# Optimization experiments

Measured on AMD Instinct MI355X. Metric: run time of the kernel, lower is better.

Reference implementation:

```python
import jax, jax.numpy as jnp
import numpy as np

CONF_THRES = 0.96
IOU_THRES = 0.45
MAX_CAND = 2048        # fixed candidate cap (jit-static stand-in for data-dependent nonzero)
DET_PER_IMG = 300
AGNOSTIC = False
LABEL_OFF = 4.0        # class offset for batched NMS; boxes lie within [-0.5, 1.5]


def _cxcywh_to_xyxy(b):
    cx, cy, w, h = b[..., 0], b[..., 1], b[..., 2], b[..., 3]
    return jnp.stack([cx - 0.5 * w, cy - 0.5 * h, cx + 0.5 * w, cy + 0.5 * h], axis=-1)


def _box_iou(a, b):
    # a: [K,4], b: [K,4] -> [K,K]
    lt = jnp.maximum(a[:, None, :2], b[None, :, :2])
    rb = jnp.minimum(a[:, None, 2:], b[None, :, 2:])
    wh = jnp.clip(rb - lt, 0.0)
    inter = wh[..., 0] * wh[..., 1]
    area_a = (a[:, 2] - a[:, 0]) * (a[:, 3] - a[:, 1])
    area_b = (b[:, 2] - b[:, 0]) * (b[:, 3] - b[:, 1])
    return inter / (area_a[:, None] + area_b[None, :] - inter + 1e-9)


def _process_image(x, nc):
    # x: [N, 5+nc]
    obj = x[:, 4]
    cls_scores = x[:, 5:] * obj[:, None]                 # x[:,5:] *= x[:,4:5]
    boxes = _cxcywh_to_xyxy(x[:, :4])                    # [N,4]
    # multi-label candidates: (obj > conf) pre-filter, then (obj*cls > conf)
    cand_mask = (cls_scores > CONF_THRES) & (obj[:, None] > CONF_THRES)
    flat_scores = jnp.where(cand_mask, cls_scores, -1.0).reshape(-1)  # [N*nc]
    top_scores, top_idx = jax.lax.top_k(flat_scores, MAX_CAND)        # sorted desc
    anchor = top_idx // nc
    label = top_idx % nc
    cand_boxes = boxes[anchor]                           # [K,4]
    valid = top_scores > 0.0

    # batched (class-aware) NMS via per-class coordinate offset
    if AGNOSTIC:
        nms_boxes = cand_boxes
    else:
        nms_boxes = cand_boxes + (label.astype(cand_boxes.dtype) * LABEL_OFF)[:, None]
    iou = _box_iou(nms_boxes, nms_boxes)                 # [K,K]
    idxs = jnp.arange(MAX_CAND)

    def body(i, keep):
        suppress = keep[i] & (iou[i] > IOU_THRES) & (idxs > i)
        return keep & ~suppress

    keep = jax.lax.fori_loop(0, MAX_CAND, body, valid)
    kept_scores = jnp.where(keep, top_scores, -1.0)
    det_scores, det_idx = jax.lax.top_k(kept_scores, DET_PER_IMG)
    det_valid = det_scores > 0.0
    det = jnp.concatenate(
        [cand_boxes[det_idx], det_scores[:, None], label[det_idx].astype(x.dtype)[:, None]],
        axis=1,
    )  # [DET_PER_IMG, 6] = (x1, y1, x2, y2, score, class)
    return jnp.where(det_valid[:, None], det, 0.0)


def setup_inputs() -> dict:
    key = jax.random.key(0)
    prediction = jax.random.uniform(key, (8, 25200, 85), dtype=jnp.float32)
    return {"prediction": prediction}


def reference(prediction):
    nc = prediction.shape[2] - 5
    return jax.vmap(lambda x: _process_image(x, nc))(prediction)
```

## Files before the change

kernel.cpp:

```cpp
#include <hip/hip_runtime.h>
#include <stdint.h>

#define CONF 0.96f
#define IOUT 0.45f
#define NA 25200
#define DIM 85
#define NC 80
#define NIMG 8
#define NCAND 2048
#define CAPRAW 4096
#define NDET 300
#define CSTRIDE 32
#define CH 64
#define NCH (NCAND / CH)
#define NTPAIR ((NCH * (NCH + 1)) / 2)

#define APB 112
#define BCAP 256
__global__ __launch_bounds__(256) void k1_filter(
    const float* __restrict__ pred, int* __restrict__ cnt,
    float* __restrict__ raw_s, int* __restrict__ raw_f) {
    __shared__ float lds[APB * DIM];
    __shared__ float l_s[BCAP];
    __shared__ int   l_f[BCAP];
    __shared__ int   l_cnt, l_base;
    int tid = threadIdx.x;
    int img = blockIdx.y;
    int a0 = blockIdx.x * APB;
    if (tid == 0) l_cnt = 0;

    const float4* src = (const float4*)(pred + ((size_t)img * NA + a0) * DIM);
    float4* dst = (float4*)lds;
    for (int i = tid; i < (APB * DIM / 4); i += 256) dst[i] = src[i];
    __syncthreads();

    for (int it = 0; it < (APB * NC / 256); ++it) {
        int w = tid + it * 256;
        int al = w / NC;
        int c = w - al * NC;
        float obj = lds[al * DIM + 4];
        float s = lds[al * DIM + 5 + c] * obj;
        if (s > CONF && obj > CONF) {
            int p = atomicAdd(&l_cnt, 1);
            if (p < BCAP) { l_s[p] = s; l_f[p] = (a0 + al) * NC + c; }
        }
    }
    __syncthreads();
    int c = l_cnt; if (c > BCAP) c = BCAP;
    if (tid == 0) l_base = c ? atomicAdd(&cnt[img * CSTRIDE], c) : 0;
    __syncthreads();
    int base = l_base;
    for (int i = tid; i < c; i += 256) {
        int pos = base + i;
        if (pos < CAPRAW) {
            raw_s[img * CAPRAW + pos] = l_s[i];
            raw_f[img * CAPRAW + pos] = l_f[i];
        }
    }
}

__global__ __launch_bounds__(256) void k2_rank(
    const float* __restrict__ pred,
    const int* __restrict__ cnt, int* __restrict__ n_arr,
    const float* __restrict__ raw_s, const int* __restrict__ raw_f,
    float* __restrict__ score, int* __restrict__ label,
    float* __restrict__ ox1, float* __restrict__ oy1,
    float* __restrict__ ox2, float* __restrict__ oy2,
    float* __restrict__ area,
    float* __restrict__ rx1, float* __restrict__ ry1,
    float* __restrict__ rx2, float* __restrict__ ry2) {
    __shared__ uint64_t keys[CAPRAW];
    int img = blockIdx.y;
    int tid = threadIdx.x;
    int m = cnt[img * CSTRIDE]; if (m > CAPRAW) m = CAPRAW;
    if (blockIdx.x == 0 && tid == 0) n_arr[img] = m < NCAND ? m : NCAND;

    const float* rs = raw_s + img * CAPRAW;
    const int*   rf = raw_f + img * CAPRAW;
    for (int j = tid; j < CAPRAW; j += 256) {
        uint64_t k = 0;
        if (j < m)
            k = ((uint64_t)__float_as_uint(rs[j]) << 32) | (uint32_t)(~(uint32_t)rf[j]);
        keys[j] = k;
    }
    __syncthreads();
    if (blockIdx.x * 256 >= m) return;

    int idx = blockIdx.x * 256 + tid;
    bool valid = idx < m;
    uint64_t my = keys[idx];
    int mt = (m + 7) & ~7;
    int rank = 0;
#pragma unroll 8
    for (int j = 0; j < mt; ++j) rank += (keys[j] > my) ? 1 : 0;

    if (valid && rank < NCAND) {
        float s = __uint_as_float((uint32_t)(my >> 32));
        uint32_t myf = ~((uint32_t)my);
        int anchor = (int)(myf / NC);
        int lab = (int)(myf - (uint32_t)anchor * NC);
        const float* p = pred + ((size_t)img * NA + anchor) * DIM;
        float cx = p[0], cy = p[1], wv = p[2], hv = p[3];
        float x1 = cx - 0.5f * wv, y1 = cy - 0.5f * hv;
        float x2 = cx + 0.5f * wv, y2 = cy + 0.5f * hv;
        float off = (float)lab * 4.0f;
        size_t o = (size_t)img * NCAND + rank;
        score[o] = s; label[o] = lab;
        rx1[o] = x1; ry1[o] = y1; rx2[o] = x2; ry2[o] = y2;
        float o1 = x1 + off, o2 = y1 + off, o3 = x2 + off, o4 = y2 + off;
        ox1[o] = o1; oy1[o] = o2; ox2[o] = o3; oy2[o] = o4;
        area[o] = (o3 - o1) * (o4 - o2);
    }
}

__global__ __launch_bounds__(64) void k3_mask(
    const int* __restrict__ n_arr,
    const float* __restrict__ ox1, const float* __restrict__ oy1,
    const float* __restrict__ ox2, const float* __restrict__ oy2,
    const float* __restrict__ area, uint64_t* __restrict__ mask64) {
    int img = blockIdx.y;
    int n = n_arr[img];
    int p = blockIdx.x, ci = 0;
    while (p >= NCH - ci) { p -= NCH - ci; ++ci; }
    int cj = ci + p;
    if (ci * CH >= n) return;
    int t = threadIdx.x;
    size_t base = (size_t)img * NCAND;
    __shared__ float jx1[CH], jy1[CH], jx2[CH], jy2[CH], jar[CH];
    {
        int j = cj * CH + t;
        float x1 = 0.f, y1 = 0.f, x2 = 0.f, y2 = 0.f, ar = 0.f;
        if (j < n) {
            x1 = ox1[base + j]; y1 = oy1[base + j];
            x2 = ox2[base + j]; y2 = oy2[base + j]; ar = area[base + j];
        }
        jx1[t] = x1; jy1[t] = y1; jx2[t] = x2; jy2[t] = y2; jar[t] = ar;
    }
    __syncthreads();
    int i = ci * CH + t;
    float ax1 = 0.f, ay1 = 0.f, ax2 = 0.f, ay2 = 0.f, aar = 0.f;
    if (i < n) {
        ax1 = ox1[base + i]; ay1 = oy1[base + i];
        ax2 = ox2[base + i]; ay2 = oy2[base + i]; aar = area[base + i];
    }
    int jg0 = cj * CH;
    uint64_t w = 0;
#pragma unroll 8
    for (int jj = 0; jj < CH; ++jj) {
        float ltx = fmaxf(ax1, jx1[jj]), lty = fmaxf(ay1, jy1[jj]);
        float rbx = fminf(ax2, jx2[jj]), rby = fminf(ay2, jy2[jj]);
        float ww = fmaxf(rbx - ltx, 0.f), hh = fmaxf(rby - lty, 0.f);
        float inter = ww * hh;
        float iou = inter / (aar + jar[jj] - inter + 1e-9f);
        w |= (iou > IOUT && (jg0 + jj) > i) ? (1ull << jj) : 0ull;
    }
    mask64[(base + (size_t)i) * NCH + cj] = w;
}

__global__ void k4_scan(const int* __restrict__ n_arr,
                        const uint32_t* __restrict__ mask,
                        const float* __restrict__ score, const int* __restrict__ label,
                        const float* __restrict__ rx1, const float* __restrict__ ry1,
                        const float* __restrict__ rx2, const float* __restrict__ ry2,
                        float* __restrict__ out) {
    int img = blockIdx.x;
    int lane = threadIdx.x;
    int n = n_arr[img];
    size_t cbase = (size_t)img * NCAND;
    const uint32_t* rowp = mask + cbase * 64 + lane;
    float* outp = out + (size_t)img * NDET * 6;

    uint32_t removed = 0;
    int kcnt = 0;
    constexpr int PF = 32;
    uint32_t buf[PF];
#pragma unroll
    for (int k = 0; k < PF; ++k) buf[k] = rowp[(size_t)k * 64];
    for (int ib = 0; ib < n; ib += PF) {
#pragma unroll
        for (int k = 0; k < PF; ++k) {
            int i = ib + k;
            uint32_t row = buf[k];
            int pi = i + PF; if (pi > NCAND - 1) pi = NCAND - 1;
            buf[k] = rowp[(size_t)pi * 64];
            uint32_t w = (uint32_t)__builtin_amdgcn_readlane((int)removed, i >> 5);
            uint32_t kept = ((w >> (i & 31)) & 1u) ^ 1u;
            kcnt += (int)kept;
            removed |= row & (0u - kept);
        }
        if (kcnt >= NDET) break;
    }

    int j0 = lane << 5;
    uint32_t vmask = (j0 + 32 <= n) ? 0xffffffffu
                   : (j0 >= n ? 0u : ((1u << (n - j0)) - 1u));
    uint32_t keptw = ~removed & vmask;
    int cnt = __popc(keptw);
    int pre = cnt;
    for (int d = 1; d < 64; d <<= 1) {
        int tv = __shfl_up(pre, d);
        if (lane >= d) pre += tv;
    }
    int total = __shfl(pre, 63);
    int r = pre - cnt;
    uint32_t wv = keptw;
    while (wv) {
        int b = __builtin_ctz(wv);
        wv &= wv - 1;
        if (r >= NDET) break;
        int j = j0 + b;
        float* o = outp + (size_t)r * 6;
        o[0] = rx1[cbase + j]; o[1] = ry1[cbase + j];
        o[2] = rx2[cbase + j]; o[3] = ry2[cbase + j];
        o[4] = score[cbase + j]; o[5] = (float)label[cbase + j];
        ++r;
    }
    int nk = total < NDET ? total : NDET;
    for (int idx = nk * 6 + lane; idx < NDET * 6; idx += 64) outp[idx] = 0.0f;
}

extern "C" void kernel_launch(void* const* d_in, const int* in_sizes, int n_in,
                              void* d_out, int out_size, void* d_ws, size_t ws_size,
                              hipStream_t stream) {
    const float* pred = (const float*)d_in[0];
    float* out = (float*)d_out;
    char* w = (char*)d_ws;

    const size_t A_CNT = 0;
    const size_t A_N   = 1024;
    const size_t A_RS  = 1280;
    const size_t SZ_RAW = (size_t)NIMG * CAPRAW * 4;
    const size_t A_RF  = A_RS + SZ_RAW;
    const size_t SA    = A_RF + SZ_RAW;
    const size_t SZ_S  = (size_t)NIMG * NCAND * 4;

    int*   cnt   = (int*)(w + A_CNT);
    int*   n_arr = (int*)(w + A_N);
    float* raw_s = (float*)(w + A_RS);
    int*   raw_f = (int*)(w + A_RF);
    float* score = (float*)(w + SA + 0 * SZ_S);
    int*   label = (int*)(w + SA + 1 * SZ_S);
    float* ox1   = (float*)(w + SA + 2 * SZ_S);
    float* oy1   = (float*)(w + SA + 3 * SZ_S);
    float* ox2   = (float*)(w + SA + 4 * SZ_S);
    float* oy2   = (float*)(w + SA + 5 * SZ_S);
    float* area  = (float*)(w + SA + 6 * SZ_S);
    float* rx1   = (float*)(w + SA + 7 * SZ_S);
    float* ry1   = (float*)(w + SA + 8 * SZ_S);
    float* rx2   = (float*)(w + SA + 9 * SZ_S);
    float* ry2   = (float*)(w + SA + 10 * SZ_S);
    uint64_t* mask64 = (uint64_t*)(w + SA + 11 * SZ_S);
    uint32_t* mask32 = (uint32_t*)mask64;

    hipMemsetAsync(cnt, 0, NIMG * CSTRIDE * sizeof(int), stream);
    hipMemsetAsync(mask64, 0, (size_t)NIMG * NCAND * NCH * 8, stream);
    dim3 g1(NA / APB, NIMG);
    k1_filter<<<g1, 256, 0, stream>>>(pred, cnt, raw_s, raw_f);
    dim3 g2(CAPRAW / 256, NIMG);
    k2_rank<<<g2, 256, 0, stream>>>(pred, cnt, n_arr, raw_s, raw_f,
        score, label, ox1, oy1, ox2, oy2, area, rx1, ry1, rx2, ry2);
    dim3 g3(NTPAIR, NIMG);
    k3_mask<<<g3, CH, 0, stream>>>(n_arr, ox1, oy1, ox2, oy2, area, mask64);
    k4_scan<<<NIMG, 64, 0, stream>>>(n_arr, mask32, score, label,
        rx1, ry1, rx2, ry2, out);
}
```

Measured before the change: 180.1 us.

## Fuse four NMS kernels into one cooperative persistent kernel with grid syncs

Merges filter, rank, IoU-mask and scan stages into a single cooperative kernel of 256 persistent blocks, separated by grid-wide syncs. Mask tiles are distributed across waves, and every tile (including inactive ones) writes zeros, which replaces the large mask memset. This targets the fixed cost of several kernel launches and one big memset. In exchange it adds grid-sync overhead, and the filter and rank stages run on fewer resident blocks than the original wide grids.

```diff
diff --git a/kernel.cpp b/kernel.cpp
--- a/kernel.cpp
+++ b/kernel.cpp
@@ -1,5 +1,7 @@
 #include <hip/hip_runtime.h>
+#include <hip/hip_cooperative_groups.h>
 #include <stdint.h>
+namespace cg = cooperative_groups;
 
 #define CONF 0.96f
 #define IOUT 0.45f
@@ -13,210 +15,221 @@
 #define CSTRIDE 32
 #define CH 64
 #define NCH (NCAND / CH)
-#define NTPAIR ((NCH * (NCH + 1)) / 2)
-
 #define APB 112
+#define NT1 (NA / APB)
 #define BCAP 256
-__global__ __launch_bounds__(256) void k1_filter(
-    const float* __restrict__ pred, int* __restrict__ cnt,
-    float* __restrict__ raw_s, int* __restrict__ raw_f) {
-    __shared__ float lds[APB * DIM];
-    __shared__ float l_s[BCAP];
-    __shared__ int   l_f[BCAP];
-    __shared__ int   l_cnt, l_base;
+#define NBLK 256
+#define NTHR 256
+
+__global__ __launch_bounds__(NTHR) void mega(
+    const float* __restrict__ pred, float* __restrict__ out,
+    int* cnt, int* n_arr, float* raw_s, int* raw_f,
+    float* score, int* label,
+    float* ox1, float* oy1, float* ox2, float* oy2, float* area,
+    float* rx1, float* ry1, float* rx2, float* ry2,
+    uint64_t* mask64) {
+    cg::grid_group grid = cg::this_grid();
+    __shared__ alignas(16) unsigned char smem[40192];
     int tid = threadIdx.x;
-    int img = blockIdx.y;
-    int a0 = blockIdx.x * APB;
-    if (tid == 0) l_cnt = 0;
-
-    const float4* src = (const float4*)(pred + ((size_t)img * NA + a0) * DIM);
-    float4* dst = (float4*)lds;
-    for (int i = tid; i < (APB * DIM / 4); i += 256) dst[i] = src[i];
-    __syncthreads();
-
-    for (int it = 0; it < (APB * NC / 256); ++it) {
-        int w = tid + it * 256;
-        int al = w / NC;
-        int c = w - al * NC;
-        float obj = lds[al * DIM + 4];
-        float s = lds[al * DIM + 5 + c] * obj;
-        if (s > CONF && obj > CONF) {
-            int p = atomicAdd(&l_cnt, 1);
-            if (p < BCAP) { l_s[p] = s; l_f[p] = (a0 + al) * NC + c; }
-        }
-    }
-    __syncthreads();
-    int c = l_cnt; if (c > BCAP) c = BCAP;
-    if (tid == 0) l_base = c ? atomicAdd(&cnt[img * CSTRIDE], c) : 0;
-    __syncthreads();
-    int base = l_base;
-    for (int i = tid; i < c; i += 256) {
-        int pos = base + i;
-        if (pos < CAPRAW) {
-            raw_s[img * CAPRAW + pos] = l_s[i];
-            raw_f[img * CAPRAW + pos] = l_f[i];
-        }
-    }
-}
-
-__global__ __launch_bounds__(256) void k2_rank(
-    const float* __restrict__ pred,
-    const int* __restrict__ cnt, int* __restrict__ n_arr,
-    const float* __restrict__ raw_s, const int* __restrict__ raw_f,
-    float* __restrict__ score, int* __restrict__ label,
-    float* __restrict__ ox1, float* __restrict__ oy1,
-    float* __restrict__ ox2, float* __restrict__ oy2,
-    float* __restrict__ area,
-    float* __restrict__ rx1, float* __restrict__ ry1,
-    float* __restrict__ rx2, float* __restrict__ ry2) {
-    __shared__ uint64_t keys[CAPRAW];
-    int img = blockIdx.y;
-    int tid = threadIdx.x;
-    int m = cnt[img * CSTRIDE]; if (m > CAPRAW) m = CAPRAW;
-    if (blockIdx.x == 0 && tid == 0) n_arr[img] = m < NCAND ? m : NCAND;
-
-    const float* rs = raw_s + img * CAPRAW;
-    const int*   rf = raw_f + img * CAPRAW;
-    for (int j = tid; j < CAPRAW; j += 256) {
-        uint64_t k = 0;
-        if (j < m)
-            k = ((uint64_t)__float_as_uint(rs[j]) << 32) | (uint32_t)(~(uint32_t)rf[j]);
-        keys[j] = k;
-    }
-    __syncthreads();
-    if (blockIdx.x * 256 >= m) return;
-
-    int idx = blockIdx.x * 256 + tid;
-    bool valid = idx < m;
-    uint64_t my = keys[idx];
-    int mt = (m + 7) & ~7;
-    int rank = 0;
+    int blk = blockIdx.x;
+
+    {
+        float* tile = (float*)smem;
+        float* l_s  = (float*)(smem + 38080);
+        int*   l_f  = (int*)  (smem + 38080 + 1024);
+        int*   l_c  = (int*)  (smem + 38080 + 2048);
+        for (int t = blk; t < NT1 * NIMG; t += NBLK) {
+            int img = t / NT1;
+            int a0 = (t - img * NT1) * APB;
+            if (tid == 0) l_c[0] = 0;
+            __syncthreads();
+            const float4* src = (const float4*)(pred + ((size_t)img * NA + a0) * DIM);
+            float4* dst = (float4*)tile;
+            for (int i = tid; i < (APB * DIM / 4); i += NTHR) dst[i] = src[i];
+            __syncthreads();
+            for (int it = 0; it < (APB * NC / NTHR); ++it) {
+                int wI = tid + it * NTHR;
+                int al = wI / NC;
+                int c  = wI - al * NC;
+                float obj = tile[al * DIM + 4];
+                float s = tile[al * DIM + 5 + c] * obj;
+                if (s > CONF && obj > CONF) {
+                    int p = atomicAdd(&l_c[0], 1);
+                    if (p < BCAP) { l_s[p] = s; l_f[p] = (a0 + al) * NC + c; }
+                }
+            }
+            __syncthreads();
+            int c = l_c[0]; if (c > BCAP) c = BCAP;
+            if (tid == 0) l_c[1] = c ? atomicAdd(&cnt[img * CSTRIDE], c) : 0;
+            __syncthreads();
+            int base = l_c[1];
+            for (int i = tid; i < c; i += NTHR) {
+                int pos = base + i;
+                if (pos < CAPRAW) {
+                    raw_s[img * CAPRAW + pos] = l_s[i];
+                    raw_f[img * CAPRAW + pos] = l_f[i];
+                }
+            }
+            __syncthreads();
+        }
+    }
+    __threadfence();
+    grid.sync();
+
+    if (blk < NIMG * (CAPRAW / NTHR)) {
+        uint64_t* keys = (uint64_t*)smem;
+        int img = blk >> 4;
+        int unit = blk & 15;
+        int m = cnt[img * CSTRIDE]; if (m > CAPRAW) m = CAPRAW;
+        if (unit == 0 && tid == 0) n_arr[img] = m < NCAND ? m : NCAND;
+        const float* rs = raw_s + img * CAPRAW;
+        const int*   rf = raw_f + img * CAPRAW;
+        for (int j = tid; j < CAPRAW; j += NTHR) {
+            uint64_t k = 0;
+            if (j < m)
+                k = ((uint64_t)__float_as_uint(rs[j]) << 32) | (uint32_t)(~(uint32_t)rf[j]);
+            keys[j] = k;
+        }
+        __syncthreads();
+        if (unit * NTHR < m) {
+            int idx = unit * NTHR + tid;
+            bool valid = idx < m;
+            uint64_t my = keys[idx];
+            int mt = (m + 7) & ~7;
+            int rank = 0;
 #pragma unroll 8
-    for (int j = 0; j < mt; ++j) rank += (keys[j] > my) ? 1 : 0;
-
-    if (valid && rank < NCAND) {
-        float s = __uint_as_float((uint32_t)(my >> 32));
-        uint32_t myf = ~((uint32_t)my);
-        int anchor = (int)(myf / NC);
-        int lab = (int)(myf - (uint32_t)anchor * NC);
-        const float* p = pred + ((size_t)img * NA + anchor) * DIM;
-        float cx = p[0], cy = p[1], wv = p[2], hv = p[3];
-        float x1 = cx - 0.5f * wv, y1 = cy - 0.5f * hv;
-        float x2 = cx + 0.5f * wv, y2 = cy + 0.5f * hv;
-        float off = (float)lab * 4.0f;
-        size_t o = (size_t)img * NCAND + rank;
-        score[o] = s; label[o] = lab;
-        rx1[o] = x1; ry1[o] = y1; rx2[o] = x2; ry2[o] = y2;
-        float o1 = x1 + off, o2 = y1 + off, o3 = x2 + off, o4 = y2 + off;
-        ox1[o] = o1; oy1[o] = o2; ox2[o] = o3; oy2[o] = o4;
-        area[o] = (o3 - o1) * (o4 - o2);
-    }
-}
-
-__global__ __launch_bounds__(64) void k3_mask(
-    const int* __restrict__ n_arr,
-    const float* __restrict__ ox1, const float* __restrict__ oy1,
-    const float* __restrict__ ox2, const float* __restrict__ oy2,
-    const float* __restrict__ area, uint64_t* __restrict__ mask64) {
-    int img = blockIdx.y;
-    int n = n_arr[img];
-    int p = blockIdx.x, ci = 0;
-    while (p >= NCH - ci) { p -= NCH - ci; ++ci; }
-    int cj = ci + p;
-    if (ci * CH >= n) return;
-    int t = threadIdx.x;
-    size_t base = (size_t)img * NCAND;
-    __shared__ float jx1[CH], jy1[CH], jx2[CH], jy2[CH], jar[CH];
+            for (int j = 0; j < mt; ++j) rank += (keys[j] > my) ? 1 : 0;
+            if (valid && rank < NCAND) {
+                float s = __uint_as_float((uint32_t)(my >> 32));
+                uint32_t myf = ~((uint32_t)my);
+                int anchor = (int)(myf / NC);
+                int lab = (int)(myf - (uint32_t)anchor * NC);
+                const float* p = pred + ((size_t)img * NA + anchor) * DIM;
+                float cx = p[0], cy = p[1], wv = p[2], hv = p[3];
+                float x1 = cx - 0.5f * wv, y1 = cy - 0.5f * hv;
+                float x2 = cx + 0.5f * wv, y2 = cy + 0.5f * hv;
+                float off = (float)lab * 4.0f;
+                size_t o = (size_t)img * NCAND + rank;
+                score[o] = s; label[o] = lab;
+                rx1[o] = x1; ry1[o] = y1; rx2[o] = x2; ry2[o] = y2;
+                float o1 = x1 + off, o2 = y1 + off, o3 = x2 + off, o4 = y2 + off;
+                ox1[o] = o1; oy1[o] = o2; ox2[o] = o3; oy2[o] = o4;
+                area[o] = (o3 - o1) * (o4 - o2);
+            }
+        }
+    }
+    __threadfence();
+    grid.sync();
+
     {
-        int j = cj * CH + t;
-        float x1 = 0.f, y1 = 0.f, x2 = 0.f, y2 = 0.f, ar = 0.f;
-        if (j < n) {
-            x1 = ox1[base + j]; y1 = oy1[base + j];
-            x2 = ox2[base + j]; y2 = oy2[base + j]; ar = area[base + j];
-        }
-        jx1[t] = x1; jy1[t] = y1; jx2[t] = x2; jy2[t] = y2; jar[t] = ar;
-    }
-    __syncthreads();
-    int i = ci * CH + t;
-    float ax1 = 0.f, ay1 = 0.f, ax2 = 0.f, ay2 = 0.f, aar = 0.f;
-    if (i < n) {
-        ax1 = ox1[base + i]; ay1 = oy1[base + i];
-        ax2 = ox2[base + i]; ay2 = oy2[base + i]; aar = area[base + i];
-    }
-    int jg0 = cj * CH;
-    uint64_t w = 0;
+        int wv = tid >> 6, lane = tid & 63;
+        float* jx1 = (float*)smem + (wv * 5 + 0) * 64;
+        float* jy1 = (float*)smem + (wv * 5 + 1) * 64;
+        float* jx2 = (float*)smem + (wv * 5 + 2) * 64;
+        float* jy2 = (float*)smem + (wv * 5 + 3) * 64;
+        float* jar = (float*)smem + (wv * 5 + 4) * 64;
+        for (int it = 0; it < 8; ++it) {
+            int T = it * (NBLK * 4) + blk * 4 + wv;
+            int img = T >> 10;
+            int r = T & 1023;
+            int ci = r >> 5, cj = r & 31;
+            int n = n_arr[img];
+            size_t base = (size_t)img * NCAND;
+            bool active = (cj >= ci) && (ci * CH < n) && (cj * CH < n);
+            if (active) {
+                int j = cj * CH + lane;
+                float x1 = 0.f, y1 = 0.f, x2 = 0.f, y2 = 0.f, ar = 0.f;
+                if (j < n) {
+                    x1 = ox1[base + j]; y1 = oy1[base + j];
+                    x2 = ox2[base + j]; y2 = oy2[base + j]; ar = area[base + j];
+                }
+                jx1[lane] = x1; jy1[lane] = y1; jx2[lane] = x2;
+                jy2[lane] = y2; jar[lane] = ar;
+            }
+            __syncthreads();
+            uint64_t w = 0;
+            int i = ci * CH + lane;
+            if (active) {
+                float ax1 = 0.f, ay1 = 0.f, ax2 = 0.f, ay2 = 0.f, aar = 0.f;
+                if (i < n) {
+                    ax1 = ox1[base + i]; ay1 = oy1[base + i];
+                    ax2 = ox2[base + i]; ay2 = oy2[base + i]; aar = area[base + i];
+                }
+                int jg0 = cj * CH;
 #pragma unroll 8
-    for (int jj = 0; jj < CH; ++jj) {
-        float ltx = fmaxf(ax1, jx1[jj]), lty = fmaxf(ay1, jy1[jj]);
-        float rbx = fminf(ax2, jx2[jj]), rby = fminf(ay2, jy2[jj]);
-        float ww = fmaxf(rbx - ltx, 0.f), hh = fmaxf(rby - lty, 0.f);
-        float inter = ww * hh;
-        float iou = inter / (aar + jar[jj] - inter + 1e-9f);
-        w |= (iou > IOUT && (jg0 + jj) > i) ? (1ull << jj) : 0ull;
-    }
-    mask64[(base + (size_t)i) * NCH + cj] = w;
-}
-
-__global__ void k4_scan(const int* __restrict__ n_arr,
-                        const uint32_t* __restrict__ mask,
-                        const float* __restrict__ score, const int* __restrict__ label,
-                        const float* __restrict__ rx1, const float* __restrict__ ry1,
-                        const float* __restrict__ rx2, const float* __restrict__ ry2,
-                        float* __restrict__ out) {
-    int img = blockIdx.x;
-    int lane = threadIdx.x;
-    int n = n_arr[img];
-    size_t cbase = (size_t)img * NCAND;
-    const uint32_t* rowp = mask + cbase * 64 + lane;
-    float* outp = out + (size_t)img * NDET * 6;
-
-    uint32_t removed = 0;
-    int kcnt = 0;
-    constexpr int PF = 32;
-    uint32_t buf[PF];
+                for (int jj = 0; jj < CH; ++jj) {
+                    float ltx = fmaxf(ax1, jx1[jj]), lty = fmaxf(ay1, jy1[jj]);
+                    float rbx = fminf(ax2, jx2[jj]), rby = fminf(ay2, jy2[jj]);
+                    float ww = fmaxf(rbx - ltx, 0.f), hh = fmaxf(rby - lty, 0.f);
+                    float inter = ww * hh;
+                    float iou = inter / (aar + jar[jj] - inter + 1e-9f);
+                    w |= (iou > IOUT && (jg0 + jj) > i) ? (1ull << jj) : 0ull;
+                }
+            }
+            mask64[(base + (size_t)i) * NCH + cj] = w;
+            __syncthreads();
+        }
+    }
+    __threadfence();
+    grid.sync();
+
+    if (blk < NIMG && tid < 64) {
+        const uint32_t* mask = (const uint32_t*)mask64;
+        int img = blk;
+        int lane = tid;
+        int n = n_arr[img];
+        size_t cbase = (size_t)img * NCAND;
+        const uint32_t* rowp = mask + cbase * 64 + lane;
+        float* outp = out + (size_t)img * NDET * 6;
+
+        uint32_t removed = 0;
+        int kcnt = 0;
+        constexpr int PF = 32;
+        uint32_t buf[PF];
 #pragma unroll
-    for (int k = 0; k < PF; ++k) buf[k] = rowp[(size_t)k * 64];
-    for (int ib = 0; ib < n; ib += PF) {
+        for (int k = 0; k < PF; ++k) buf[k] = rowp[(size_t)k * 64];
+        for (int ib = 0; ib < n; ib += PF) {
 #pragma unroll
-        for (int k = 0; k < PF; ++k) {
-            int i = ib + k;
-            uint32_t row = buf[k];
-            int pi = i + PF; if (pi > NCAND - 1) pi = NCAND - 1;
-            buf[k] = rowp[(size_t)pi * 64];
-            uint32_t w = (uint32_t)__builtin_amdgcn_readlane((int)removed, i >> 5);
-            uint32_t kept = ((w >> (i & 31)) & 1u) ^ 1u;
-            kcnt += (int)kept;
-            removed |= row & (0u - kept);
-        }
-        if (kcnt >= NDET) break;
-    }
-
-    int j0 = lane << 5;
-    uint32_t vmask = (j0 + 32 <= n) ? 0xffffffffu
-                   : (j0 >= n ? 0u : ((1u << (n - j0)) - 1u));
-    uint32_t keptw = ~removed & vmask;
-    int cnt = __popc(keptw);
-    int pre = cnt;
-    for (int d = 1; d < 64; d <<= 1) {
-        int tv = __shfl_up(pre, d);
-        if (lane >= d) pre += tv;
-    }
-    int total = __shfl(pre, 63);
-    int r = pre - cnt;
-    uint32_t wv = keptw;
-    while (wv) {
-        int b = __builtin_ctz(wv);
-        wv &= wv - 1;
-        if (r >= NDET) break;
-        int j = j0 + b;
-        float* o = outp + (size_t)r * 6;
-        o[0] = rx1[cbase + j]; o[1] = ry1[cbase + j];
-        o[2] = rx2[cbase + j]; o[3] = ry2[cbase + j];
-        o[4] = score[cbase + j]; o[5] = (float)label[cbase + j];
-        ++r;
-    }
-    int nk = total < NDET ? total : NDET;
-    for (int idx = nk * 6 + lane; idx < NDET * 6; idx += 64) outp[idx] = 0.0f;
+            for (int k = 0; k < PF; ++k) {
+                int i = ib + k;
+                uint32_t row = buf[k];
+                int pi = i + PF; if (pi > NCAND - 1) pi = NCAND - 1;
+                buf[k] = rowp[(size_t)pi * 64];
+                uint32_t w = (uint32_t)__builtin_amdgcn_readlane((int)removed, i >> 5);
+                uint32_t kept = ((w >> (i & 31)) & 1u) ^ 1u;
+                kcnt += (int)kept;
+                removed |= row & (0u - kept);
+            }
+            if (kcnt >= NDET) break;
+        }
+
+        int j0 = lane << 5;
+        uint32_t vmask = (j0 + 32 <= n) ? 0xffffffffu
+                       : (j0 >= n ? 0u : ((1u << (n - j0)) - 1u));
+        uint32_t keptw = ~removed & vmask;
+        int cntk = __popc(keptw);
+        int pre = cntk;
+        for (int d = 1; d < 64; d <<= 1) {
+            int tv = __shfl_up(pre, d);
+            if (lane >= d) pre += tv;
+        }
+        int total = __shfl(pre, 63);
+        int r = pre - cntk;
+        uint32_t wvb = keptw;
+        while (wvb) {
+            int b = __builtin_ctz(wvb);
+            wvb &= wvb - 1;
+            if (r >= NDET) break;
+            int j = j0 + b;
+            float* o = outp + (size_t)r * 6;
+            o[0] = rx1[cbase + j]; o[1] = ry1[cbase + j];
+            o[2] = rx2[cbase + j]; o[3] = ry2[cbase + j];
+            o[4] = score[cbase + j]; o[5] = (float)label[cbase + j];
+            ++r;
+        }
+        int nk = total < NDET ? total : NDET;
+        for (int idx = nk * 6 + lane; idx < NDET * 6; idx += 64) outp[idx] = 0.0f;
+    }
 }
 
 extern "C" void kernel_launch(void* const* d_in, const int* in_sizes, int n_in,
@@ -250,17 +263,15 @@
     float* rx2   = (float*)(w + SA + 9 * SZ_S);
     float* ry2   = (float*)(w + SA + 10 * SZ_S);
     uint64_t* mask64 = (uint64_t*)(w + SA + 11 * SZ_S);
-    uint32_t* mask32 = (uint32_t*)mask64;
 
     hipMemsetAsync(cnt, 0, NIMG * CSTRIDE * sizeof(int), stream);
-    hipMemsetAsync(mask64, 0, (size_t)NIMG * NCAND * NCH * 8, stream);
-    dim3 g1(NA / APB, NIMG);
-    k1_filter<<<g1, 256, 0, stream>>>(pred, cnt, raw_s, raw_f);
-    dim3 g2(CAPRAW / 256, NIMG);
-    k2_rank<<<g2, 256, 0, stream>>>(pred, cnt, n_arr, raw_s, raw_f,
-        score, label, ox1, oy1, ox2, oy2, area, rx1, ry1, rx2, ry2);
-    dim3 g3(NTPAIR, NIMG);
-    k3_mask<<<g3, CH, 0, stream>>>(n_arr, ox1, oy1, ox2, oy2, area, mask64);
-    k4_scan<<<NIMG, 64, 0, stream>>>(n_arr, mask32, score, label,
-        rx1, ry1, rx2, ry2, out);
+
+    void* args[] = {
+        (void*)&pred, (void*)&out, (void*)&cnt, (void*)&n_arr,
+        (void*)&raw_s, (void*)&raw_f, (void*)&score, (void*)&label,
+        (void*)&ox1, (void*)&oy1, (void*)&ox2, (void*)&oy2, (void*)&area,
+        (void*)&rx1, (void*)&ry1, (void*)&rx2, (void*)&ry2, (void*)&mask64,
+    };
+    hipLaunchCooperativeKernel((const void*)mega, dim3(NBLK), dim3(NTHR),
+                               args, 0, stream);
 }
```

Result: slower. 372.5 us (+106.9%).

## Prefilter anchors by objectness and write full mask grid instead of memset

Applied to the files above, without the earlier changes.

The filter kernel first collects anchors whose objectness exceeds the threshold, then scores classes only for those anchors, skipping most per-class multiply-compare work. The IoU mask kernel now launches the full square tile grid and writes zeros for tiles that are below the diagonal or out of range, so the separate memset of the mask buffer is removed. The trade-off is more (mostly trivial) blocks in the mask kernel, plus an extra shared-memory atomic phase and barrier in the filter kernel.

```diff
diff --git a/kernel.cpp b/kernel.cpp
--- a/kernel.cpp
+++ b/kernel.cpp
@@ -13,34 +13,41 @@
 #define CSTRIDE 32
 #define CH 64
 #define NCH (NCAND / CH)
-#define NTPAIR ((NCH * (NCH + 1)) / 2)
 
 #define APB 112
 #define BCAP 256
 __global__ __launch_bounds__(256) void k1_filter(
     const float* __restrict__ pred, int* __restrict__ cnt,
     float* __restrict__ raw_s, int* __restrict__ raw_f) {
-    __shared__ float lds[APB * DIM];
+    __shared__ float tile[APB * DIM];
+    __shared__ int   hot[APB];
     __shared__ float l_s[BCAP];
     __shared__ int   l_f[BCAP];
-    __shared__ int   l_cnt, l_base;
+    __shared__ int   l_hot, l_cnt, l_base;
     int tid = threadIdx.x;
     int img = blockIdx.y;
     int a0 = blockIdx.x * APB;
-    if (tid == 0) l_cnt = 0;
+    if (tid == 0) { l_hot = 0; l_cnt = 0; }
 
     const float4* src = (const float4*)(pred + ((size_t)img * NA + a0) * DIM);
-    float4* dst = (float4*)lds;
+    float4* dst = (float4*)tile;
     for (int i = tid; i < (APB * DIM / 4); i += 256) dst[i] = src[i];
     __syncthreads();
 
-    for (int it = 0; it < (APB * NC / 256); ++it) {
-        int w = tid + it * 256;
-        int al = w / NC;
-        int c = w - al * NC;
-        float obj = lds[al * DIM + 4];
-        float s = lds[al * DIM + 5 + c] * obj;
-        if (s > CONF && obj > CONF) {
+    if (tid < APB) {
+        float obj = tile[tid * DIM + 4];
+        if (obj > CONF) { int p = atomicAdd(&l_hot, 1); hot[p] = tid; }
+    }
+    __syncthreads();
+    int nh = l_hot;
+    int items = nh * NC;
+    for (int w = tid; w < items; w += 256) {
+        int hi = w / NC;
+        int c = w - hi * NC;
+        int al = hot[hi];
+        float obj = tile[al * DIM + 4];
+        float s = tile[al * DIM + 5 + c] * obj;
+        if (s > CONF) {
             int p = atomicAdd(&l_cnt, 1);
             if (p < BCAP) { l_s[p] = s; l_f[p] = (a0 + al) * NC + c; }
         }
@@ -118,41 +125,40 @@
     const float* __restrict__ ox1, const float* __restrict__ oy1,
     const float* __restrict__ ox2, const float* __restrict__ oy2,
     const float* __restrict__ area, uint64_t* __restrict__ mask64) {
+    __shared__ float jx1[CH], jy1[CH], jx2[CH], jy2[CH], jar[CH];
     int img = blockIdx.y;
     int n = n_arr[img];
-    int p = blockIdx.x, ci = 0;
-    while (p >= NCH - ci) { p -= NCH - ci; ++ci; }
-    int cj = ci + p;
-    if (ci * CH >= n) return;
+    int ci = blockIdx.x >> 5, cj = blockIdx.x & 31;
     int t = threadIdx.x;
     size_t base = (size_t)img * NCAND;
-    __shared__ float jx1[CH], jy1[CH], jx2[CH], jy2[CH], jar[CH];
-    {
-        int j = cj * CH + t;
-        float x1 = 0.f, y1 = 0.f, x2 = 0.f, y2 = 0.f, ar = 0.f;
-        if (j < n) {
-            x1 = ox1[base + j]; y1 = oy1[base + j];
-            x2 = ox2[base + j]; y2 = oy2[base + j]; ar = area[base + j];
-        }
-        jx1[t] = x1; jy1[t] = y1; jx2[t] = x2; jy2[t] = y2; jar[t] = ar;
-    }
-    __syncthreads();
     int i = ci * CH + t;
-    float ax1 = 0.f, ay1 = 0.f, ax2 = 0.f, ay2 = 0.f, aar = 0.f;
-    if (i < n) {
-        ax1 = ox1[base + i]; ay1 = oy1[base + i];
-        ax2 = ox2[base + i]; ay2 = oy2[base + i]; aar = area[base + i];
-    }
-    int jg0 = cj * CH;
     uint64_t w = 0;
+    if (cj >= ci && ci * CH < n && cj * CH < n) {
+        {
+            int j = cj * CH + t;
+            float x1 = 0.f, y1 = 0.f, x2 = 0.f, y2 = 0.f, ar = 0.f;
+            if (j < n) {
+                x1 = ox1[base + j]; y1 = oy1[base + j];
+                x2 = ox2[base + j]; y2 = oy2[base + j]; ar = area[base + j];
+            }
+            jx1[t] = x1; jy1[t] = y1; jx2[t] = x2; jy2[t] = y2; jar[t] = ar;
+        }
+        __syncthreads();
+        float ax1 = 0.f, ay1 = 0.f, ax2 = 0.f, ay2 = 0.f, aar = 0.f;
+        if (i < n) {
+            ax1 = ox1[base + i]; ay1 = oy1[base + i];
+            ax2 = ox2[base + i]; ay2 = oy2[base + i]; aar = area[base + i];
+        }
+        int jg0 = cj * CH;
 #pragma unroll 8
-    for (int jj = 0; jj < CH; ++jj) {
-        float ltx = fmaxf(ax1, jx1[jj]), lty = fmaxf(ay1, jy1[jj]);
-        float rbx = fminf(ax2, jx2[jj]), rby = fminf(ay2, jy2[jj]);
-        float ww = fmaxf(rbx - ltx, 0.f), hh = fmaxf(rby - lty, 0.f);
-        float inter = ww * hh;
-        float iou = inter / (aar + jar[jj] - inter + 1e-9f);
-        w |= (iou > IOUT && (jg0 + jj) > i) ? (1ull << jj) : 0ull;
+        for (int jj = 0; jj < CH; ++jj) {
+            float ltx = fmaxf(ax1, jx1[jj]), lty = fmaxf(ay1, jy1[jj]);
+            float rbx = fminf(ax2, jx2[jj]), rby = fminf(ay2, jy2[jj]);
+            float ww = fmaxf(rbx - ltx, 0.f), hh = fmaxf(rby - lty, 0.f);
+            float inter = ww * hh;
+            float iou = inter / (aar + jar[jj] - inter + 1e-9f);
+            w |= (iou > IOUT && (jg0 + jj) > i) ? (1ull << jj) : 0ull;
+        }
     }
     mask64[(base + (size_t)i) * NCH + cj] = w;
 }
@@ -195,14 +201,14 @@
     uint32_t vmask = (j0 + 32 <= n) ? 0xffffffffu
                    : (j0 >= n ? 0u : ((1u << (n - j0)) - 1u));
     uint32_t keptw = ~removed & vmask;
-    int cnt = __popc(keptw);
-    int pre = cnt;
+    int cntk = __popc(keptw);
+    int pre = cntk;
     for (int d = 1; d < 64; d <<= 1) {
         int tv = __shfl_up(pre, d);
         if (lane >= d) pre += tv;
     }
     int total = __shfl(pre, 63);
-    int r = pre - cnt;
+    int r = pre - cntk;
     uint32_t wv = keptw;
     while (wv) {
         int b = __builtin_ctz(wv);
@@ -253,13 +259,12 @@
     uint32_t* mask32 = (uint32_t*)mask64;
 
     hipMemsetAsync(cnt, 0, NIMG * CSTRIDE * sizeof(int), stream);
-    hipMemsetAsync(mask64, 0, (size_t)NIMG * NCAND * NCH * 8, stream);
     dim3 g1(NA / APB, NIMG);
     k1_filter<<<g1, 256, 0, stream>>>(pred, cnt, raw_s, raw_f);
     dim3 g2(CAPRAW / 256, NIMG);
     k2_rank<<<g2, 256, 0, stream>>>(pred, cnt, n_arr, raw_s, raw_f,
         score, label, ox1, oy1, ox2, oy2, area, rx1, ry1, rx2, ry2);
-    dim3 g3(NTPAIR, NIMG);
+    dim3 g3(NCH * NCH, NIMG);
     k3_mask<<<g3, CH, 0, stream>>>(n_arr, ox1, oy1, ox2, oy2, area, mask64);
     k4_scan<<<NIMG, 64, 0, stream>>>(n_arr, mask32, score, label,
         rx1, ry1, rx2, ry2, out);
```

Result: no change. 182.5 us (+1.4%).
